# Optimization experiments

Measured on AMD Instinct MI355X. Metric: run time of the kernel, lower is better.

Reference implementation:

```python
import jax, jax.numpy as jnp
import numpy as np

B, S, D, E, R = 1024, 20, 128, 128, 8
NU, NI = 100000, 100000
ALPHA = 0.5


def setup_inputs() -> dict:
    key = jax.random.key(0)
    ks = jax.random.split(key, 10)
    return {
        "users_ids": jax.random.randint(ks[0], (B,), 0, NU),
        "users_items": jax.random.randint(ks[1], (B, S), 0, NI),
        "users_rewards": jax.random.uniform(ks[2], (B, S), dtype=jnp.float32),
        "step_num": S,
        "items_table": jax.random.normal(ks[3], (NI, D), dtype=jnp.float32) * 0.02,
        "users_memory": jax.random.normal(ks[4], (NU, D), dtype=jnp.float32) * 0.02,
        "items_memory": jax.random.normal(ks[5], (NI, D), dtype=jnp.float32) * 0.02,
        "Wx": jax.random.normal(ks[6], (3 * D, D + R), dtype=jnp.float32) * 0.05,
        "Wh": jax.random.normal(ks[7], (3 * D, D), dtype=jnp.float32) * 0.05,
        "bx": jnp.zeros((3 * D,), jnp.float32),
        "bh": jnp.zeros((3 * D,), jnp.float32),
        "W_u": jax.random.normal(ks[8], (D, E), dtype=jnp.float32) * 0.05,
        "W_i": jax.random.normal(ks[9], (D, E), dtype=jnp.float32) * 0.05,
    }


def _gru(x, Wx, Wh, bx, bh):
    # x: [B,S,I]; torch GRU gate order (r, z, n). Precompute input projections.
    gx = jnp.einsum('bsi,gi->sbg', x, Wx) + bx  # [S,B,3D]
    h0 = jnp.zeros((x.shape[0], D), x.dtype)

    def step(h, gxt):
        gh = h @ Wh.T + bh
        r = jax.nn.sigmoid(gxt[:, :D] + gh[:, :D])
        z = jax.nn.sigmoid(gxt[:, D:2 * D] + gh[:, D:2 * D])
        n = jnp.tanh(gxt[:, 2 * D:] + r * gh[:, 2 * D:])
        h_new = (1.0 - z) * n + z * h
        return h_new, h_new

    hT, seq = jax.lax.scan(step, h0, gx)
    return jnp.transpose(seq, (1, 0, 2)), hT  # [B,S,D], [B,D]


def reference(users_ids, users_items, users_rewards, step_num, items_table,
              users_memory, items_memory, Wx, Wh, bx, bh, W_u, W_i):
    items_seq = users_items[:, :step_num]                      # [B,S]
    raw = items_table[items_seq]                               # gather [B,S,D]
    rew = jnp.repeat(users_rewards[:, :step_num, None], R, axis=-1)
    x = jnp.concatenate([raw, rew], axis=-1)                   # [B,S,D+R]
    seq_h, hT = _gru(x, Wx, Wh, bx, bh)
    # set_memory: overwrite users' memory with final GRU state
    users_memory = users_memory.at[users_ids].set(hT)
    # unique+index_add mean aggregation == segment mean over flat item ids
    flat = items_seq.reshape(-1)
    sums = jax.ops.segment_sum(seq_h.reshape(-1, D), flat, num_segments=NI)
    counts = jax.ops.segment_sum(jnp.ones_like(flat, dtype=seq_h.dtype), flat,
                                 num_segments=NI)
    mean = sums / jnp.maximum(counts, 1.0)[:, None]
    touched = (counts > 0)[:, None]
    # update_memory: EMA blend only for items seen in this batch
    items_memory = jnp.where(touched,
                             ALPHA * items_memory + (1.0 - ALPHA) * mean,
                             items_memory)
    # embedding module inputs: users 'memory', items 'sum'
    items_input = items_memory + items_table
    users_emb = users_memory[users_ids] @ W_u                  # [B,E]
    items_emb = items_input @ W_i                              # [NI,E]
    return users_emb @ items_emb.T                             # [B,NI]
```

## Files before the change

### kernel.cpp

```cpp
#include <hip/hip_runtime.h>
#include <hip/hip_bf16.h>
#include <stdint.h>

#define BB  1024
#define SS  20
#define DD  128
#define G3  384
#define NII 100000
#define KXX 136
#define RPB 2

typedef float  f32x4  __attribute__((ext_vector_type(4)));
typedef __bf16 bf16x8 __attribute__((ext_vector_type(8)));

__device__ __forceinline__ unsigned short f2bf(float x) {
  uint32_t u = __float_as_uint(x);
  uint32_t r = (u + 0x7fffu + ((u >> 16) & 1u)) >> 16;
  return (unsigned short)r;
}

__device__ __forceinline__ float sigf(float x) { return 1.f / (1.f + expf(-x)); }

__global__ __launch_bounds__(256) void k_zero_seg(const int* __restrict__ items,
                                                  float* __restrict__ sums,
                                                  float* __restrict__ counts) {
  int tid = blockIdx.x * 256 + threadIdx.x;
  int p = tid >> 5, c = tid & 31;
  if (p >= BB * SS) return;
  int it = items[p];
  f32x4 z = {0.f, 0.f, 0.f, 0.f};
  *(f32x4*)(sums + (size_t)it * DD + c * 4) = z;
  if (c == 0) counts[it] = 0.f;
}

__global__ __launch_bounds__(256) void k_M(const float* __restrict__ Wu,
                                           const float* __restrict__ Wi,
                                           float* __restrict__ M) {
  int idx = blockIdx.x * 256 + threadIdx.x;
  int k1 = idx >> 7, k2 = idx & 127;
  float acc = 0.f;
  for (int e = 0; e < DD; ++e)
    acc = fmaf(Wu[k1 * DD + e], Wi[k2 * DD + e], acc);
  M[idx] = acc;
}

__global__ __launch_bounds__(256) void k_gx(const int* __restrict__ items,
                                            const float* __restrict__ rew,
                                            const float* __restrict__ table,
                                            const float* __restrict__ Wx,
                                            const float* __restrict__ bx,
                                            float* __restrict__ gx) {
  __shared__ float Wl[96][140];
  __shared__ float Al[32][128];
  __shared__ float rl[32];
  int gt = blockIdx.x & 3, pt = blockIdx.x >> 2;
  int g0 = gt * 96, p0 = pt * 32;
  int t = threadIdx.x;
  for (int i = t; i < 96 * 34; i += 256) {
    int r = i / 34, c = i % 34;
    f32x4 v = *(const f32x4*)(Wx + (size_t)(g0 + r) * KXX + c * 4);
    *(f32x4*)&Wl[r][c * 4] = v;
  }
  for (int i = t; i < 32 * 32; i += 256) {
    int r = i >> 5, c = i & 31;
    int it = items[p0 + r];
    *(f32x4*)&Al[r][c * 4] = *(const f32x4*)(table + (size_t)it * DD + c * 4);
  }
  if (t < 32) rl[t] = rew[p0 + t];
  __syncthreads();

  int tg = t & 31, pq = t >> 5;
  float acc[4][3] = {};
  for (int k4 = 0; k4 < 32; ++k4) {
    f32x4 a[4];
#pragma unroll
    for (int i = 0; i < 4; ++i) a[i] = *(f32x4*)&Al[pq + 8 * i][k4 * 4];
#pragma unroll
    for (int u = 0; u < 3; ++u) {
      f32x4 w = *(f32x4*)&Wl[tg + 32 * u][k4 * 4];
#pragma unroll
      for (int i = 0; i < 4; ++i)
        acc[i][u] += a[i].x * w.x + a[i].y * w.y + a[i].z * w.z + a[i].w * w.w;
    }
  }
#pragma unroll
  for (int u = 0; u < 3; ++u) {
    int gl = tg + 32 * u, g = g0 + gl;
    float wxr = 0.f;
#pragma unroll
    for (int q = 0; q < 8; ++q) wxr += Wl[gl][128 + q];
    float bxv = bx[g];
#pragma unroll
    for (int i = 0; i < 4; ++i) {
      int p = p0 + pq + 8 * i;
      gx[(size_t)p * G3 + g] = acc[i][u] + rl[pq + 8 * i] * wxr + bxv;
    }
  }
}

__global__ __launch_bounds__(256, 2) void k_gru(const float* __restrict__ gx,
                                                const float* __restrict__ Wh,
                                                const float* __restrict__ bh,
                                                const int* __restrict__ items,
                                                float* __restrict__ sums,
                                                float* __restrict__ counts,
                                                float* __restrict__ hT) {
  __shared__ float hl[RPB][DD];
  __shared__ float ghl[RPB][G3];
  int t = threadIdx.x;
  int gbase = t >> 1, half = t & 1;

  f32x4 wreg[3][16];
#pragma unroll
  for (int tt = 0; tt < 3; ++tt) {
    const float* src = Wh + (size_t)(tt * 128 + gbase) * DD + half * 64;
#pragma unroll
    for (int j4 = 0; j4 < 16; ++j4)
      wreg[tt][j4] = *(const f32x4*)(src + j4 * 4);
  }

  int u2 = t >> 7, w2 = t & 127;
  float bh3[3];
#pragma unroll
  for (int q = 0; q < 3; ++q) bh3[q] = bh[q * 128 + w2];

  int b0 = blockIdx.x * RPB;
  const float* gxb = gx + (size_t)(b0 + u2) * SS * G3;
  const int*   itb = items + (b0 + u2) * SS;
  hl[u2][w2] = 0.f;
  float hcur = 0.f;
  __syncthreads();

  for (int s = 0; s < SS; ++s) {
    float g3[3];
#pragma unroll
    for (int q = 0; q < 3; ++q) g3[q] = gxb[s * G3 + q * 128 + w2];
    int it = itb[s];

#pragma unroll
    for (int r = 0; r < RPB; ++r) {
      float a0 = 0.f, a1 = 0.f, a2 = 0.f;
#pragma unroll
      for (int j4 = 0; j4 < 16; ++j4) {
        f32x4 hv = *(f32x4*)&hl[r][half * 64 + j4 * 4];
        a0 += wreg[0][j4].x * hv.x + wreg[0][j4].y * hv.y
            + wreg[0][j4].z * hv.z + wreg[0][j4].w * hv.w;
        a1 += wreg[1][j4].x * hv.x + wreg[1][j4].y * hv.y
            + wreg[1][j4].z * hv.z + wreg[1][j4].w * hv.w;
        a2 += wreg[2][j4].x * hv.x + wreg[2][j4].y * hv.y
            + wreg[2][j4].z * hv.z + wreg[2][j4].w * hv.w;
      }
      a0 += __shfl_xor(a0, 1);
      a1 += __shfl_xor(a1, 1);
      a2 += __shfl_xor(a2, 1);
      if (!half) {
        ghl[r][gbase]       = a0;
        ghl[r][128 + gbase] = a1;
        ghl[r][256 + gbase] = a2;
      }
    }
    __syncthreads();
    float rr = sigf(g3[0] + ghl[u2][w2]       + bh3[0]);
    float zz = sigf(g3[1] + ghl[u2][128 + w2] + bh3[1]);
    float nn = tanhf(g3[2] + rr * (ghl[u2][256 + w2] + bh3[2]));
    hcur = (1.f - zz) * nn + zz * hcur;
    hl[u2][w2] = hcur;
    atomicAdd(sums + (size_t)it * DD + w2, hcur);
    if (w2 == 0) atomicAdd(counts + it, 1.f);
    __syncthreads();
  }
  hT[(b0 + u2) * DD + w2] = hcur;
}

__global__ __launch_bounds__(256) void k_items(const float* __restrict__ table,
                                               const float* __restrict__ mem,
                                               const float* __restrict__ sums,
                                               const float* __restrict__ counts,
                                               unsigned short* __restrict__ Ibf) {
  size_t tid = (size_t)blockIdx.x * 256 + threadIdx.x;
  size_t i = tid >> 5; int c = (int)(tid & 31);
  if (i >= NII) return;
  float cnt = counts[i];
  size_t base = i * DD + c * 4;
  f32x4 m  = *(const f32x4*)(mem + base);
  f32x4 tb = *(const f32x4*)(table + base);
  float vx, vy, vz, vw;
  if (cnt > 0.f) {
    f32x4 sm = *(const f32x4*)(sums + base);
    vx = 0.5f * (m.x + sm.x / cnt) + tb.x;
    vy = 0.5f * (m.y + sm.y / cnt) + tb.y;
    vz = 0.5f * (m.z + sm.z / cnt) + tb.z;
    vw = 0.5f * (m.w + sm.w / cnt) + tb.w;
  } else {
    vx = m.x + tb.x; vy = m.y + tb.y; vz = m.z + tb.z; vw = m.w + tb.w;
  }
  unsigned long long pack = (unsigned long long)f2bf(vx)
                          | ((unsigned long long)f2bf(vy) << 16)
                          | ((unsigned long long)f2bf(vz) << 32)
                          | ((unsigned long long)f2bf(vw) << 48);
  *(unsigned long long*)(Ibf + base) = pack;
}

__global__ __launch_bounds__(256) void k_uprime(const int* __restrict__ ids,
                                                const float* __restrict__ hT,
                                                const float* __restrict__ M,
                                                unsigned short* __restrict__ Ubf) {
  __shared__ int   idsl[BB];
  __shared__ int   repl[16][16];
  __shared__ float hTl[16][DD];
  int t = threadIdx.x;
  for (int i = t; i < BB; i += 256) idsl[i] = ids[i];
  __syncthreads();
  int b0 = blockIdx.x * 16;
  int p = t >> 4, c = t & 15;
  int myid = idsl[b0 + p];
  int best = -1;
  for (int j = c * 64; j < c * 64 + 64; ++j)
    if (idsl[j] == myid) best = j;
  repl[p][c] = best;
  __syncthreads();
  if (c == 0) {
    int rr = -1;
#pragma unroll
    for (int q = 0; q < 16; ++q) rr = max(rr, repl[p][q]);
    repl[p][0] = rr;
  }
  __syncthreads();
  for (int i = t; i < 16 * 32; i += 256) {
    int rr = i >> 5, c4 = i & 31;
    int src = repl[rr][0];
    *(f32x4*)&hTl[rr][c4 * 4] = *(const f32x4*)(hT + (size_t)src * DD + c4 * 4);
  }
  __syncthreads();
  float acc[8] = {0.f, 0.f, 0.f, 0.f, 0.f, 0.f, 0.f, 0.f};
  for (int k1 = 0; k1 < DD; ++k1) {
    float hv = hTl[p][k1];
#pragma unroll
    for (int u = 0; u < 8; ++u)
      acc[u] = fmaf(hv, M[k1 * DD + c + 16 * u], acc[u]);
  }
#pragma unroll
  for (int u = 0; u < 8; ++u)
    Ubf[(size_t)(b0 + p) * DD + c + 16 * u] = f2bf(acc[u]);
}

__device__ __forceinline__ bf16x8 bzero8() {
  bf16x8 z;
#pragma unroll
  for (int e = 0; e < 8; ++e) z[e] = (__bf16)0.f;
  return z;
}

__global__ __launch_bounds__(256) void k_gemm(const unsigned short* __restrict__ Ubf,
                                              const unsigned short* __restrict__ Ibf,
                                              float* __restrict__ out) {
  int j0 = blockIdx.x * 64;
  int t = threadIdx.x;
  int wv = t >> 6, l = t & 63;
  int wr = wv >> 1, wc = wv & 1;
  int jw = j0 + wc * 32;
  int lr = l & 15, lk = l >> 4;

  bf16x8 afrag[4][2];
  int ja0 = jw + lr, ja1 = jw + 16 + lr;
#pragma unroll
  for (int kk = 0; kk < 4; ++kk) {
    int k0 = kk * 32 + lk * 8;
    afrag[kk][0] = (ja0 < NII) ? *(const bf16x8*)(Ibf + (size_t)ja0 * DD + k0) : bzero8();
    afrag[kk][1] = (ja1 < NII) ? *(const bf16x8*)(Ibf + (size_t)ja1 * DD + k0) : bzero8();
  }
  int jb0 = jw + lk * 4;
  bool v0 = (jb0 < NII), v1 = (jb0 + 16 < NII);

  for (int bc = 0; bc < 16; ++bc) {
    int bw = bc * 64 + wr * 32;
    f32x4 acc[2][2];
#pragma unroll
    for (int ji = 0; ji < 2; ++ji)
#pragma unroll
      for (int bi = 0; bi < 2; ++bi) { f32x4 z = {0.f,0.f,0.f,0.f}; acc[ji][bi] = z; }

#pragma unroll
    for (int kk = 0; kk < 4; ++kk) {
      int k0 = kk * 32 + lk * 8;
      bf16x8 b0 = *(const bf16x8*)(Ubf + (size_t)(bw + lr) * DD + k0);
      bf16x8 b1 = *(const bf16x8*)(Ubf + (size_t)(bw + 16 + lr) * DD + k0);
      acc[0][0] = __builtin_amdgcn_mfma_f32_16x16x32_bf16(afrag[kk][0], b0, acc[0][0], 0, 0, 0);
      acc[0][1] = __builtin_amdgcn_mfma_f32_16x16x32_bf16(afrag[kk][0], b1, acc[0][1], 0, 0, 0);
      acc[1][0] = __builtin_amdgcn_mfma_f32_16x16x32_bf16(afrag[kk][1], b0, acc[1][0], 0, 0, 0);
      acc[1][1] = __builtin_amdgcn_mfma_f32_16x16x32_bf16(afrag[kk][1], b1, acc[1][1], 0, 0, 0);
    }
#pragma unroll
    for (int ji = 0; ji < 2; ++ji) {
      if (ji ? v1 : v0) {
        int jb = jw + ji * 16 + lk * 4;
#pragma unroll
        for (int bi = 0; bi < 2; ++bi) {
          int bb = bw + bi * 16 + lr;
          *(f32x4*)(out + (size_t)bb * NII + jb) = acc[ji][bi];
        }
      }
    }
  }
}

extern "C" void kernel_launch(void* const* d_in, const int* in_sizes, int n_in,
                              void* d_out, int out_size, void* d_ws, size_t ws_size,
                              hipStream_t stream) {
  const int*   users_ids   = (const int*)  d_in[0];
  const int*   users_items = (const int*)  d_in[1];
  const float* users_rew   = (const float*)d_in[2];
  const float* items_table = (const float*)d_in[4];
  const float* items_mem   = (const float*)d_in[6];
  const float* Wx  = (const float*)d_in[7];
  const float* Wh  = (const float*)d_in[8];
  const float* bx  = (const float*)d_in[9];
  const float* bh  = (const float*)d_in[10];
  const float* W_u = (const float*)d_in[11];
  const float* W_i = (const float*)d_in[12];
  float* out = (float*)d_out;
  (void)in_sizes; (void)n_in; (void)out_size; (void)ws_size;

  char* ws = (char*)d_ws;
  size_t off = 0;
  auto alloc = [&](size_t bytes) {
    void* p = ws + off;
    off = (off + bytes + 255) & ~(size_t)255;
    return p;
  };
  float* sums   = (float*)alloc(sizeof(float) * (size_t)NII * DD);
  float* counts = (float*)alloc(sizeof(float) * NII);
  float* gx     = (float*)alloc(sizeof(float) * (size_t)BB * SS * G3);
  float* M      = (float*)alloc(sizeof(float) * DD * DD);
  float* hT     = (float*)alloc(sizeof(float) * BB * DD);
  unsigned short* Ubf = (unsigned short*)alloc(sizeof(unsigned short) * BB * DD);
  unsigned short* Ibf = (unsigned short*)alloc(sizeof(unsigned short) * (size_t)NII * DD);

  hipLaunchKernelGGL(k_zero_seg, dim3((BB * SS * 32) / 256), dim3(256), 0, stream,
                     users_items, sums, counts);
  hipLaunchKernelGGL(k_M, dim3(64), dim3(256), 0, stream, W_u, W_i, M);
  hipLaunchKernelGGL(k_gx, dim3((BB * SS / 32) * 4), dim3(256), 0, stream,
                     users_items, users_rew, items_table, Wx, bx, gx);
  hipLaunchKernelGGL(k_gru, dim3(BB / RPB), dim3(256), 0, stream,
                     gx, Wh, bh, users_items, sums, counts, hT);
  hipLaunchKernelGGL(k_items, dim3((NII * 32 + 255) / 256), dim3(256), 0, stream,
                     items_table, items_mem, sums, counts, Ibf);
  hipLaunchKernelGGL(k_uprime, dim3(BB / 16), dim3(256), 0, stream,
                     users_ids, hT, M, Ubf);
  hipLaunchKernelGGL(k_gemm, dim3((NII + 63) / 64), dim3(256), 0, stream,
                     Ubf, Ibf, out);
}
```

Before: 331.1 us.

## Widen GEMM item tile and stage output through LDS for coalesced row stores

Each GEMM block now covers 256 items instead of 64, with every wave holding 64 item rows of fragments and computing a 64x64 tile per user chunk. This cuts the number of times the user fragments are reloaded. Accumulators are transposed through a shared-memory buffer so each wave writes full 1 KB contiguous output row segments instead of scattered 16-byte pieces. The cost is more registers, about 66 KB of LDS per block, two barriers per chunk, and fewer blocks (391), which may underfill the GPU.

```diff
diff --git a/kernel.cpp b/kernel.cpp
--- a/kernel.cpp
+++ b/kernel.cpp
@@ -9,6 +9,7 @@
 #define NII 100000
 #define KXX 136
 #define RPB 2
+#define JPB 256
 
 typedef float  f32x4  __attribute__((ext_vector_type(4)));
 typedef __bf16 bf16x8 __attribute__((ext_vector_type(8)));
@@ -251,54 +252,64 @@
   return z;
 }
 
-__global__ __launch_bounds__(256) void k_gemm(const unsigned short* __restrict__ Ubf,
-                                              const unsigned short* __restrict__ Ibf,
-                                              float* __restrict__ out) {
-  int j0 = blockIdx.x * 64;
+__global__ __launch_bounds__(256, 2) void k_gemm(const unsigned short* __restrict__ Ubf,
+                                                 const unsigned short* __restrict__ Ibf,
+                                                 float* __restrict__ out) {
+  __shared__ float ldsT[64][JPB + 4];
+  int j0 = blockIdx.x * JPB;
   int t = threadIdx.x;
   int wv = t >> 6, l = t & 63;
-  int wr = wv >> 1, wc = wv & 1;
-  int jw = j0 + wc * 32;
+  int jw = j0 + wv * 64;
   int lr = l & 15, lk = l >> 4;
 
-  bf16x8 afrag[4][2];
-  int ja0 = jw + lr, ja1 = jw + 16 + lr;
-#pragma unroll
-  for (int kk = 0; kk < 4; ++kk) {
-    int k0 = kk * 32 + lk * 8;
-    afrag[kk][0] = (ja0 < NII) ? *(const bf16x8*)(Ibf + (size_t)ja0 * DD + k0) : bzero8();
-    afrag[kk][1] = (ja1 < NII) ? *(const bf16x8*)(Ibf + (size_t)ja1 * DD + k0) : bzero8();
-  }
-  int jb0 = jw + lk * 4;
-  bool v0 = (jb0 < NII), v1 = (jb0 + 16 < NII);
-
-  for (int bc = 0; bc < 16; ++bc) {
-    int bw = bc * 64 + wr * 32;
-    f32x4 acc[2][2];
-#pragma unroll
-    for (int ji = 0; ji < 2; ++ji)
-#pragma unroll
-      for (int bi = 0; bi < 2; ++bi) { f32x4 z = {0.f,0.f,0.f,0.f}; acc[ji][bi] = z; }
-
+  bf16x8 afrag[4][4];
+#pragma unroll
+  for (int ji = 0; ji < 4; ++ji) {
+    int ja = jw + ji * 16 + lr;
 #pragma unroll
     for (int kk = 0; kk < 4; ++kk) {
       int k0 = kk * 32 + lk * 8;
-      bf16x8 b0 = *(const bf16x8*)(Ubf + (size_t)(bw + lr) * DD + k0);
-      bf16x8 b1 = *(const bf16x8*)(Ubf + (size_t)(bw + 16 + lr) * DD + k0);
-      acc[0][0] = __builtin_amdgcn_mfma_f32_16x16x32_bf16(afrag[kk][0], b0, acc[0][0], 0, 0, 0);
-      acc[0][1] = __builtin_amdgcn_mfma_f32_16x16x32_bf16(afrag[kk][0], b1, acc[0][1], 0, 0, 0);
-      acc[1][0] = __builtin_amdgcn_mfma_f32_16x16x32_bf16(afrag[kk][1], b0, acc[1][0], 0, 0, 0);
-      acc[1][1] = __builtin_amdgcn_mfma_f32_16x16x32_bf16(afrag[kk][1], b1, acc[1][1], 0, 0, 0);
-    }
-#pragma unroll
-    for (int ji = 0; ji < 2; ++ji) {
-      if (ji ? v1 : v0) {
-        int jb = jw + ji * 16 + lk * 4;
-#pragma unroll
-        for (int bi = 0; bi < 2; ++bi) {
-          int bb = bw + bi * 16 + lr;
-          *(f32x4*)(out + (size_t)bb * NII + jb) = acc[ji][bi];
-        }
+      afrag[ji][kk] = (ja < NII) ? *(const bf16x8*)(Ibf + (size_t)ja * DD + k0) : bzero8();
+    }
+  }
+  int jcl = l * 4;
+  bool svalid = (j0 + jcl + 4 <= NII);
+
+  for (int bc = 0; bc < 16; ++bc) {
+    int bw = bc * 64;
+    f32x4 acc[4][4];
+#pragma unroll
+    for (int ji = 0; ji < 4; ++ji)
+#pragma unroll
+      for (int bi = 0; bi < 4; ++bi) { f32x4 z = {0.f,0.f,0.f,0.f}; acc[ji][bi] = z; }
+
+#pragma unroll
+    for (int kk = 0; kk < 4; ++kk) {
+      int k0 = kk * 32 + lk * 8;
+#pragma unroll
+      for (int bi = 0; bi < 4; ++bi) {
+        bf16x8 bfr = *(const bf16x8*)(Ubf + (size_t)(bw + bi * 16 + lr) * DD + k0);
+#pragma unroll
+        for (int ji = 0; ji < 4; ++ji)
+          acc[ji][bi] = __builtin_amdgcn_mfma_f32_16x16x32_bf16(afrag[ji][kk], bfr,
+                                                                acc[ji][bi], 0, 0, 0);
+      }
+    }
+    __syncthreads();
+#pragma unroll
+    for (int ji = 0; ji < 4; ++ji) {
+      int jl = wv * 64 + ji * 16 + lk * 4;
+#pragma unroll
+      for (int bi = 0; bi < 4; ++bi)
+        *(f32x4*)&ldsT[bi * 16 + lr][jl] = acc[ji][bi];
+    }
+    __syncthreads();
+    if (svalid) {
+#pragma unroll
+      for (int rr = 0; rr < 16; ++rr) {
+        int row = rr * 4 + wv;
+        f32x4 v = *(f32x4*)&ldsT[row][jcl];
+        *(f32x4*)(out + (size_t)(bw + row) * NII + j0 + jcl) = v;
       }
     }
   }
@@ -347,6 +358,6 @@
                      items_table, items_mem, sums, counts, Ibf);
   hipLaunchKernelGGL(k_uprime, dim3(BB / 16), dim3(256), 0, stream,
                      users_ids, hT, M, Ubf);
-  hipLaunchKernelGGL(k_gemm, dim3((NII + 63) / 64), dim3(256), 0, stream,
+  hipLaunchKernelGGL(k_gemm, dim3((NII + JPB - 1) / JPB), dim3(256), 0, stream,
                      Ubf, Ibf, out);
 }
```

After: 281.6 us. 15.0% less time.
